# Optimization experiments

Hardware: AMD Instinct MI355X
Metric: run time of the kernel (lower is better)

The kernel has to match this reference:

```python
import jax, jax.numpy as jnp
import numpy as np
from functools import partial

STRIDE = 32
NUM_CLASSES = 20
CONF_THRESH = 0.01
NMS_THRESH = 0.5
H = W = 96
C = 512


def setup_inputs() -> dict:
    key = jax.random.key(0)
    ks = jax.random.split(key, 6)
    cls_feat = jax.random.normal(ks[0], (1, C, H, W), dtype=jnp.float32)
    reg_feat = jax.random.normal(ks[1], (1, C, H, W), dtype=jnp.float32)
    # small init scale so sigmoid/exp stay in a realistic range
    obj_w = jax.random.normal(ks[2], (1, C), dtype=jnp.float32) * 0.05
    cls_w = jax.random.normal(ks[3], (NUM_CLASSES, C), dtype=jnp.float32) * 0.05
    reg_w = jax.random.normal(ks[4], (4, C), dtype=jnp.float32) * 0.05
    obj_b = jnp.zeros((1,), jnp.float32)
    cls_b = jnp.zeros((NUM_CLASSES,), jnp.float32)
    reg_b = jnp.zeros((4,), jnp.float32)
    return {"cls_feat": cls_feat, "reg_feat": reg_feat,
            "obj_w": obj_w, "obj_b": obj_b,
            "cls_w": cls_w, "cls_b": cls_b,
            "reg_w": reg_w, "reg_b": reg_b}


def _decode_and_score(cls_feat, reg_feat, obj_w, obj_b, cls_w, cls_b, reg_w, reg_b):
    # 1x1 convs == per-pixel matmul; permute(0,2,3,1).flatten(1,2), take batch 0
    _, _, h, w = cls_feat.shape
    obj = jnp.einsum('bchw,oc->bhwo', cls_feat, obj_w)[0].reshape(h * w, 1) + obj_b
    cls = jnp.einsum('bchw,oc->bhwo', cls_feat, cls_w)[0].reshape(h * w, NUM_CLASSES) + cls_b
    reg = jnp.einsum('bchw,oc->bhwo', reg_feat, reg_w)[0].reshape(h * w, 4) + reg_b
    scores_all = jax.nn.sigmoid(obj) * jax.nn.sigmoid(cls)            # [N, 20]
    # decode_boxes: grid of (x, y) cell coords, stride 32
    gy, gx = jnp.meshgrid(jnp.arange(h), jnp.arange(w), indexing='ij')
    grid = jnp.stack([gx, gy], axis=-1).reshape(-1, 2).astype(jnp.float32)
    ctr = (jax.nn.sigmoid(reg[:, :2]) + grid) * STRIDE               # [N, 2]
    wh = jnp.exp(reg[:, 2:]) * STRIDE                                # [N, 2]
    bboxes = jnp.concatenate([ctr - 0.5 * wh, ctr + 0.5 * wh], axis=-1)  # x1y1x2y2
    return bboxes, scores_all


@jax.jit
def reference(cls_feat, reg_feat, obj_w, obj_b, cls_w, cls_b, reg_w, reg_b):
    bboxes, scores_all = _decode_and_score(
        cls_feat, reg_feat, obj_w, obj_b, cls_w, cls_b, reg_w, reg_b)
    n = bboxes.shape[0]
    labels = jnp.argmax(scores_all, axis=1)                          # [N]
    scores = jnp.max(scores_all, axis=1)                             # [N]
    valid = scores >= CONF_THRESH
    # sort by score descending (invalid boxes pushed last)
    order = jnp.argsort(-jnp.where(valid, scores, -jnp.inf))
    b = bboxes[order]
    lab_s = labels[order]
    valid_s = valid[order]
    x1, y1, x2, y2 = b[:, 0], b[:, 1], b[:, 2], b[:, 3]
    areas = (x2 - x1) * (y2 - y1)
    # pairwise IoU, matching the numpy nms (1e-10 clamp on w/h)
    iw = jnp.maximum(1e-10, jnp.minimum(x2[:, None], x2[None, :]) - jnp.maximum(x1[:, None], x1[None, :]))
    ih = jnp.maximum(1e-10, jnp.minimum(y2[:, None], y2[None, :]) - jnp.maximum(y1[:, None], y1[None, :]))
    inter = iw * ih
    iou = inter / (areas[:, None] + areas[None, :] - inter)
    same_cls = lab_s[:, None] == lab_s[None, :]
    supp = (iou > NMS_THRESH) & same_cls                             # [N, N] suppression graph
    idx = jnp.arange(n)
    # greedy per-class NMS in score order: box i is kept iff no earlier
    # kept box of the same class has IoU > thresh with it
    def body(i, keep):
        suppressed = jnp.any(keep & supp[:, i] & (idx < i))
        return keep.at[i].set(valid_s[i] & ~suppressed)
    keep_s = jax.lax.fori_loop(0, n, body, jnp.zeros(n, dtype=bool))
    keep = jnp.zeros(n, dtype=bool).at[order].set(keep_s)            # unsort
    return bboxes, scores, labels, keep


if __name__ == '__main__':
    out = reference(**setup_inputs())
    print([o.shape for o in out], int(out[3].sum()))
```

## Files before the change

### kernel.cpp

```cpp
#include <hip/hip_runtime.h>

#define HW 9216
#define WIDTH 96
#define NCLS 20
#define NOUT 25
#define CAP 1024
#define NW 16

__global__ __launch_bounds__(256) void decode_kernel(
    const float* __restrict__ cls_feat, const float* __restrict__ reg_feat,
    const float* __restrict__ obj_w, const float* __restrict__ obj_b,
    const float* __restrict__ cls_w, const float* __restrict__ cls_b,
    const float* __restrict__ reg_w, const float* __restrict__ reg_b,
    float* __restrict__ out, unsigned* __restrict__ cnt,
    unsigned long long* __restrict__ keys)
{
    __shared__ float lds[512 * 28];
    const int tid = threadIdx.x;

    for (int i = tid; i < 25 * 512; i += 256) {
        int o = i >> 9, c = i & 511;
        float v;
        if (o == 0)        v = obj_w[c];
        else if (o < 21)   v = cls_w[(o - 1) * 512 + c];
        else               v = reg_w[(o - 21) * 512 + c];
        lds[c * 28 + o] = v;
    }
    __syncthreads();

    const int posL  = tid & 31;
    const int chunk = tid >> 5;
    const int p     = blockIdx.x * 32 + posL;
    const int cb    = chunk * 64;

    float acc[NOUT];
#pragma unroll
    for (int o = 0; o < NOUT; ++o) acc[o] = 0.f;

    const float* cf = cls_feat + cb * HW + p;
    const float* rf = reg_feat + cb * HW + p;

#pragma unroll 4
    for (int k = 0; k < 64; ++k) {
        float f = cf[k * HW];
        float g = rf[k * HW];
        const float4* w = (const float4*)(lds + (cb + k) * 28);
        float4 w0 = w[0], w1 = w[1], w2 = w[2], w3 = w[3], w4v = w[4], w5 = w[5], w6 = w[6];
        acc[0]  += f * w0.x;  acc[1]  += f * w0.y;  acc[2]  += f * w0.z;  acc[3]  += f * w0.w;
        acc[4]  += f * w1.x;  acc[5]  += f * w1.y;  acc[6]  += f * w1.z;  acc[7]  += f * w1.w;
        acc[8]  += f * w2.x;  acc[9]  += f * w2.y;  acc[10] += f * w2.z;  acc[11] += f * w2.w;
        acc[12] += f * w3.x;  acc[13] += f * w3.y;  acc[14] += f * w3.z;  acc[15] += f * w3.w;
        acc[16] += f * w4v.x; acc[17] += f * w4v.y; acc[18] += f * w4v.z; acc[19] += f * w4v.w;
        acc[20] += f * w5.x;
        acc[21] += g * w5.y;  acc[22] += g * w5.z;  acc[23] += g * w5.w;  acc[24] += g * w6.x;
    }

    __syncthreads();
    float* part = lds;
#pragma unroll
    for (int o = 0; o < NOUT; ++o) part[(chunk * 32 + posL) * NOUT + o] = acc[o];
    __syncthreads();

    float* dots = lds + 8 * 32 * NOUT;
    for (int t = tid; t < 32 * NOUT; t += 256) {
        int pos = t / NOUT, o = t - pos * NOUT;
        float s = 0.f;
#pragma unroll
        for (int c2 = 0; c2 < 8; ++c2) s += part[(c2 * 32 + pos) * NOUT + o];
        dots[t] = s;
    }
    __syncthreads();

    if (tid < 32) {
        const int pos = tid;
        const int pp  = blockIdx.x * 32 + pos;
        const float* d = dots + pos * NOUT;

        float obj  = d[0] + obj_b[0];
        float best = d[1] + cls_b[0];
        int   bk   = 0;
#pragma unroll
        for (int k = 1; k < NCLS; ++k) {
            float v = d[1 + k] + cls_b[k];
            if (v > best) { best = v; bk = k; }
        }
        float sobj  = 1.f / (1.f + expf(-obj));
        float scls  = 1.f / (1.f + expf(-best));
        float score = sobj * scls;

        float r0 = d[21] + reg_b[0], r1 = d[22] + reg_b[1];
        float r2 = d[23] + reg_b[2], r3 = d[24] + reg_b[3];
        float gx = (float)(pp % WIDTH), gy = (float)(pp / WIDTH);
        float cx = (1.f / (1.f + expf(-r0)) + gx) * 32.f;
        float cy = (1.f / (1.f + expf(-r1)) + gy) * 32.f;
        float bw = expf(r2) * 32.f;
        float bh = expf(r3) * 32.f;
        float hx = 0.5f * bw, hy = 0.5f * bh;

        ((float4*)out)[pp] = make_float4(cx - hx, cy - hy, cx + hx, cy + hy);
        out[HW * 4 + pp] = score;
        out[HW * 5 + pp] = (float)bk;
        out[HW * 6 + pp] = 0.f;

        if (score >= 0.01f) {
            unsigned slot = atomicAdd(&cnt[bk], 1u);
            if (slot < CAP) {
                unsigned sb = __float_as_uint(score) ^ 0xffffffffu;
                keys[bk * CAP + slot] = ((unsigned long long)sb << 32) | (unsigned)pp;
            }
        }
    }
}

__global__ __launch_bounds__(512) void sort_kernel(
    const unsigned* __restrict__ cnt, unsigned long long* __restrict__ keys)
{
    __shared__ unsigned long long a[CAP];
    const int c = blockIdx.x, t = threadIdx.x;
    unsigned m = cnt[c]; if (m > CAP) m = CAP;

    for (int i = t; i < CAP; i += 512)
        a[i] = (i < (int)m) ? keys[c * CAP + i] : 0xFFFFFFFFFFFFFFFFull;
    __syncthreads();

    for (int k = 2; k <= CAP; k <<= 1) {
        for (int j = k >> 1; j > 0; j >>= 1) {
            int i = ((t & ~(j - 1)) << 1) | (t & (j - 1));
            int p = i | j;
            unsigned long long x = a[i], y = a[p];
            bool up = ((i & k) == 0);
            if ((x > y) == up) { a[i] = y; a[p] = x; }
            __syncthreads();
        }
    }
    for (int i = t; i < (int)m; i += 512) keys[c * CAP + i] = a[i];
}

__global__ __launch_bounds__(1024) void build_kernel(
    const unsigned* __restrict__ cnt, const unsigned long long* __restrict__ keys,
    const float* __restrict__ bboxes, unsigned long long* __restrict__ mask)
{
    __shared__ float4 box[CAP];
    const int c = blockIdx.x >> 4, tile = blockIdx.x & 15;
    const int tid = threadIdx.x, wave = tid >> 6, lane = tid & 63;
    int m = (int)cnt[c]; if (m > CAP) m = CAP;
    const int rbase = tile << 6;
    if (rbase >= m) return;

    if (tid < m) {
        unsigned idx = (unsigned)(keys[c * CAP + tid] & 0xffffffffu);
        box[tid] = ((const float4*)bboxes)[idx];
    } else {
        box[tid] = make_float4(0.f, 0.f, 0.f, 0.f);
    }
    __syncthreads();

    unsigned long long* mrow = mask + (size_t)c * CAP * NW;
#pragma unroll 4
    for (int j = 0; j < 64; ++j) {
        const int row = rbase + (wave << 2) + (j >> 4);
        const int w   = j & 15;
        const float4 bi = box[row];
        const float4 bj = box[(w << 6) + lane];
        const float ai = (bi.z - bi.x) * (bi.w - bi.y);
        const float aj = (bj.z - bj.x) * (bj.w - bj.y);
        float iw = fminf(bi.z, bj.z) - fmaxf(bi.x, bj.x);
        float ih = fminf(bi.w, bj.w) - fmaxf(bi.y, bj.y);
        iw = fmaxf(iw, 1e-10f);
        ih = fmaxf(ih, 1e-10f);
        const float inter = iw * ih;
        const float iou = inter / (ai + aj - inter);
        unsigned long long word =
            __ballot((row < m) && (((w << 6) + lane) < m) && (iou > 0.5f));
        if (lane == 0) mrow[row * NW + w] = word;
    }
}

__device__ __forceinline__ unsigned long long uread64(unsigned long long v, int srclane) {
    unsigned lo = __builtin_amdgcn_readlane((unsigned)v, srclane);
    unsigned hi = __builtin_amdgcn_readlane((unsigned)(v >> 32), srclane);
    return ((unsigned long long)hi << 32) | lo;
}

__global__ __launch_bounds__(64) void sweep_kernel(
    const unsigned* __restrict__ cnt, const unsigned long long* __restrict__ keys,
    const unsigned long long* __restrict__ mask, float* __restrict__ keep)
{
    __shared__ unsigned lidx[CAP];
    const int c = blockIdx.x, lane = threadIdx.x;
    int m = (int)cnt[c]; if (m > CAP) m = CAP;
    const int nw = (m + 63) >> 6;
    const unsigned long long* mrow = mask + (size_t)c * CAP * NW;

    for (int j = lane; j < m; j += 64)
        lidx[j] = (unsigned)(keys[c * CAP + j] & 0xffffffffu);
    __syncthreads();

    unsigned long long remw = 0;
    for (int w = 0; w < nw; ++w) {
        const int i0 = w << 6;
        const int nb = min(64, m - i0);

        unsigned long long myrow = (lane < nb) ? mrow[(i0 + lane) * NW + w] : 0ull;
        unsigned long long cur  = uread64(remw, w);
        unsigned long long kept = 0;
#pragma unroll
        for (int b = 0; b < 64; ++b) {
            unsigned long long v = uread64(myrow, b);
            unsigned long long alive = ((cur >> b) & 1ull) ^ 1ull;
            kept |= alive << b;
            cur |= v & (0ull - alive);
        }
        if (nb < 64) kept &= (1ull << nb) - 1ull;

        if (lane < nb && ((kept >> lane) & 1ull))
            keep[lidx[i0 + lane]] = 1.0f;

        if (lane < nw) {
            unsigned long long k2 = kept, acc = remw;
            while (k2) {
                int b = __builtin_ctzll(k2);
                acc |= mrow[(i0 + b) * NW + lane];
                k2 &= k2 - 1;
            }
            remw = acc;
        }
    }
}

extern "C" void kernel_launch(void* const* d_in, const int* in_sizes, int n_in,
                              void* d_out, int out_size, void* d_ws, size_t ws_size,
                              hipStream_t stream)
{
    const float* cls_feat = (const float*)d_in[0];
    const float* reg_feat = (const float*)d_in[1];
    const float* obj_w    = (const float*)d_in[2];
    const float* obj_b    = (const float*)d_in[3];
    const float* cls_w    = (const float*)d_in[4];
    const float* cls_b    = (const float*)d_in[5];
    const float* reg_w    = (const float*)d_in[6];
    const float* reg_b    = (const float*)d_in[7];

    float* out = (float*)d_out;
    unsigned* cnt = (unsigned*)d_ws;
    unsigned long long* keys = (unsigned long long*)((char*)d_ws + 256);
    unsigned long long* mask = (unsigned long long*)((char*)d_ws + 256 + NCLS * CAP * 8);

    hipMemsetAsync(d_ws, 0, 256, stream);

    decode_kernel<<<288, 256, 0, stream>>>(cls_feat, reg_feat, obj_w, obj_b,
                                           cls_w, cls_b, reg_w, reg_b,
                                           out, cnt, keys);
    sort_kernel<<<NCLS, 512, 0, stream>>>(cnt, keys);
    build_kernel<<<NCLS * 16, 1024, 0, stream>>>(cnt, keys, out, mask);
    sweep_kernel<<<NCLS, 64, 0, stream>>>(cnt, keys, mask, out + HW * 6);
}
```

Baseline: 228.3 us.

## Parallelize NMS sweep row-OR across all lanes and drop LDS index staging

The sweep kernel used to accumulate the removal mask serially: only lanes below nw took part, each walking the kept bits with a dependent global load per bit. Now all 64 lanes prefetch 16 mask words each (a 4-row by 16-word layout) before the 64-bit greedy scan. They OR in the words for kept rows and reduce across lanes with xor shuffles. Box indices are read straight from keys per block instead of staged in LDS behind a barrier. This removes the serial latency chain at the cost of more unconditional global loads and registers per lane.

```diff
diff --git a/kernel.cpp b/kernel.cpp
--- a/kernel.cpp
+++ b/kernel.cpp
@@ -182,26 +182,42 @@
     return ((unsigned long long)hi << 32) | lo;
 }
 
+__device__ __forceinline__ unsigned long long shflxor64(unsigned long long v, int m) {
+    unsigned lo = __shfl_xor((unsigned)v, m, 64);
+    unsigned hi = __shfl_xor((unsigned)(v >> 32), m, 64);
+    return ((unsigned long long)hi << 32) | lo;
+}
+
 __global__ __launch_bounds__(64) void sweep_kernel(
     const unsigned* __restrict__ cnt, const unsigned long long* __restrict__ keys,
     const unsigned long long* __restrict__ mask, float* __restrict__ keep)
 {
-    __shared__ unsigned lidx[CAP];
     const int c = blockIdx.x, lane = threadIdx.x;
     int m = (int)cnt[c]; if (m > CAP) m = CAP;
     const int nw = (m + 63) >> 6;
     const unsigned long long* mrow = mask + (size_t)c * CAP * NW;
 
-    for (int j = lane; j < m; j += 64)
-        lidx[j] = (unsigned)(keys[c * CAP + j] & 0xffffffffu);
-    __syncthreads();
+    const int wsel = lane & 15;
+    const int rof  = lane >> 4;
 
     unsigned long long remw = 0;
     for (int w = 0; w < nw; ++w) {
         const int i0 = w << 6;
         const int nb = min(64, m - i0);
 
-        unsigned long long myrow = (lane < nb) ? mrow[(i0 + lane) * NW + w] : 0ull;
+        unsigned long long mykey =
+            (lane < nb) ? keys[c * CAP + i0 + lane] : 0ull;
+        unsigned long long myrow =
+            (lane < nb) ? mrow[(size_t)(i0 + lane) * NW + w] : 0ull;
+
+        unsigned long long rw[16];
+#pragma unroll
+        for (int j = 0; j < 16; ++j) {
+            const int r = i0 + rof + (j << 2);
+            rw[j] = (r < m && wsel < nw)
+                        ? mrow[(size_t)r * NW + wsel] : 0ull;
+        }
+
         unsigned long long cur  = uread64(remw, w);
         unsigned long long kept = 0;
 #pragma unroll
@@ -214,17 +230,17 @@
         if (nb < 64) kept &= (1ull << nb) - 1ull;
 
         if (lane < nb && ((kept >> lane) & 1ull))
-            keep[lidx[i0 + lane]] = 1.0f;
-
-        if (lane < nw) {
-            unsigned long long k2 = kept, acc = remw;
-            while (k2) {
-                int b = __builtin_ctzll(k2);
-                acc |= mrow[(i0 + b) * NW + lane];
-                k2 &= k2 - 1;
-            }
-            remw = acc;
-        }
+            keep[(unsigned)(mykey & 0xffffffffu)] = 1.0f;
+
+        unsigned long long part = 0;
+#pragma unroll
+        for (int j = 0; j < 16; ++j) {
+            const int b = rof + (j << 2);
+            part |= rw[j] & (0ull - ((kept >> b) & 1ull));
+        }
+        part |= shflxor64(part, 16);
+        part |= shflxor64(part, 32);
+        if (lane < NW) remw |= part;
     }
 }
 
```

After: 187.5 us. 1.22x faster.
